# Optimization experiments

Measured on AMD Instinct MI355X. Metric: run time of the kernel, lower is better.

## Reference

```python
import jax, jax.numpy as jnp
import numpy as np

D_MODEL = 1024
H = 16
D_K = D_MODEL // H
D_FF = 4096
EPS = 1e-6
NEG = -1e9


def layer_norm(x, alpha, beta):
    # Custom LN: scalar alpha/beta, unbiased std, eps added to std (not var)
    mean = jnp.mean(x, axis=-1, keepdims=True)
    std = jnp.std(x, axis=-1, ddof=1, keepdims=True)
    return alpha * (x - mean) / (std + EPS) + beta


def setup_inputs() -> dict:
    key = jax.random.key(0)
    ks = jax.random.split(key, 16)
    B, S = 4, 2048
    s = 1.0 / np.sqrt(D_MODEL)
    inp = {
        "x": jax.random.normal(ks[0], (B, S, D_MODEL), dtype=jnp.float32),
        "src_mask": jax.random.randint(ks[1], (B, 1, 1, S), 0, 2, dtype=jnp.int32),
        "wq": jax.random.normal(ks[2], (D_MODEL, D_MODEL), jnp.float32) * s,
        "bq": jnp.zeros((D_MODEL,), jnp.float32),
        "wk": jax.random.normal(ks[3], (D_MODEL, D_MODEL), jnp.float32) * s,
        "bk": jnp.zeros((D_MODEL,), jnp.float32),
        "wv": jax.random.normal(ks[4], (D_MODEL, D_MODEL), jnp.float32) * s,
        "bv": jnp.zeros((D_MODEL,), jnp.float32),
        "wo": jax.random.normal(ks[5], (D_MODEL, D_MODEL), jnp.float32) * s,
        "bo": jnp.zeros((D_MODEL,), jnp.float32),
        "w1": jax.random.normal(ks[6], (D_MODEL, D_FF), jnp.float32) * s,
        "b1": jnp.zeros((D_FF,), jnp.float32),
        "w2": jax.random.normal(ks[7], (D_FF, D_MODEL), jnp.float32) * (1.0 / np.sqrt(D_FF)),
        "b2": jnp.zeros((D_MODEL,), jnp.float32),
        "a1": jnp.ones((1,), jnp.float32),
        "be1": jnp.zeros((1,), jnp.float32),
        "a2": jnp.ones((1,), jnp.float32),
        "be2": jnp.zeros((1,), jnp.float32),
    }
    return inp


def reference(x, src_mask, wq, bq, wk, bk, wv, bv, wo, bo, w1, b1, w2, b2, a1, be1, a2, be2):
    B, S, _ = x.shape

    # --- residual 1: self-attention on pre-LN input (dropout = identity, eval) ---
    xn = layer_norm(x, a1, be1)
    q = (xn @ wq + bq).reshape(B, S, H, D_K).transpose(0, 2, 1, 3)  # [B,H,S,Dk]
    k = (xn @ wk + bk).reshape(B, S, H, D_K).transpose(0, 2, 1, 3)
    v = (xn @ wv + bv).reshape(B, S, H, D_K).transpose(0, 2, 1, 3)

    scores = jnp.einsum("bhqd,bhkd->bhqk", q, k) / jnp.sqrt(jnp.float32(D_K))
    scores = jnp.where(src_mask == 0, jnp.float32(NEG), scores)
    attn = jax.nn.softmax(scores, axis=-1)
    ctx = jnp.einsum("bhqk,bhkd->bhqd", attn, v)  # [B,H,S,Dk]
    ctx = ctx.transpose(0, 2, 1, 3).reshape(B, S, D_MODEL)
    attn_out = ctx @ wo + bo
    x = x + attn_out

    # --- residual 2: feed-forward on pre-LN input ---
    xn2 = layer_norm(x, a2, be2)
    ff = jax.nn.relu(xn2 @ w1 + b1) @ w2 + b2
    return x + ff
```

## Files before the change

### kernel.cpp

```cpp
#include <hip/hip_runtime.h>
#include <stdint.h>

typedef unsigned short u16;
typedef __attribute__((ext_vector_type(8))) short short8;
typedef __attribute__((ext_vector_type(4))) float f32x4;
typedef __attribute__((ext_vector_type(4))) u16 u16x4;
typedef __attribute__((ext_vector_type(4))) uint32_t u32x4;

#define NB 4
#define SEQ 2048
#define DM 1024
#define NH 16
#define DKh 64
#define DFF 4096
#define LOG2E 1.44269504089f

__device__ __forceinline__ u16 f2bf(float f) {
  union { float f; uint32_t u; } v; v.f = f;
  uint32_t u = v.u;
  return (u16)((u + 0x7FFFu + ((u >> 16) & 1u)) >> 16);
}

__device__ __forceinline__ uint32_t cvtpk(float lo, float hi) {
  uint32_t r;
  asm("v_cvt_pk_bf16_f32 %0, %1, %2" : "=v"(r) : "v"(lo), "v"(hi));
  return r;
}

__device__ __forceinline__ float fexp2(float x) {
  float r;
  asm("v_exp_f32 %0, %1" : "=v"(r) : "v"(x));
  return r;
}

__device__ __forceinline__ void gl16(const u16* g, u16* l) {
  __builtin_amdgcn_global_load_lds((const __attribute__((address_space(1))) void*)g,
                                   (__attribute__((address_space(3))) void*)l, 16, 0, 0);
}

__global__ __launch_bounds__(256) void transpose4_bf16(const float* __restrict__ s0,
                                                       const float* __restrict__ s1,
                                                       const float* __restrict__ s2,
                                                       const float* __restrict__ s3,
                                                       u16* __restrict__ d0,
                                                       u16* __restrict__ d1,
                                                       u16* __restrict__ d2,
                                                       u16* __restrict__ d3) {
  __shared__ float tile[32][33];
  int z = blockIdx.z;
  const float* src = (z == 0) ? s0 : (z == 1) ? s1 : (z == 2) ? s2 : s3;
  u16* dst = (z == 0) ? d0 : (z == 1) ? d1 : (z == 2) ? d2 : d3;
  int tx = threadIdx.x, ty = threadIdx.y;
  int c0 = blockIdx.x * 32, r0 = blockIdx.y * 32;
#pragma unroll
  for (int i = 0; i < 32; i += 8)
    tile[ty + i][tx] = src[(size_t)(r0 + ty + i) * DM + c0 + tx];
  __syncthreads();
#pragma unroll
  for (int i = 0; i < 32; i += 8)
    dst[(size_t)(c0 + ty + i) * DM + r0 + tx] = f2bf(tile[tx][ty + i]);
}

__global__ __launch_bounds__(256) void transpose_bf16(const float* __restrict__ src,
                                                      u16* __restrict__ dst, int R, int C) {
  __shared__ float tile[32][33];
  int tx = threadIdx.x, ty = threadIdx.y;
  int c0 = blockIdx.x * 32, r0 = blockIdx.y * 32;
#pragma unroll
  for (int i = 0; i < 32; i += 8)
    tile[ty + i][tx] = src[(size_t)(r0 + ty + i) * C + c0 + tx];
  __syncthreads();
#pragma unroll
  for (int i = 0; i < 32; i += 8)
    dst[(size_t)(c0 + ty + i) * R + r0 + tx] = f2bf(tile[tx][ty + i]);
}

__global__ __launch_bounds__(256) void bias_cat(const float* __restrict__ bq,
                                                const float* __restrict__ bk,
                                                const float* __restrict__ bv,
                                                float* __restrict__ o) {
  int i = blockIdx.x * 256 + threadIdx.x;
  if (i < 3072) o[i] = (i < 1024) ? bq[i] : ((i < 2048) ? bk[i - 1024] : bv[i - 2048]);
}

__global__ __launch_bounds__(1024) void compact_idx(const int* __restrict__ msk,
                                                    int* __restrict__ pinv,
                                                    int* __restrict__ lArr,
                                                    int* __restrict__ lpArr,
                                                    float* __restrict__ fbbc) {
  int b = blockIdx.x;
  int t = threadIdx.x;
  int lane = t & 63, w = t >> 6;
  int i0 = t * 2, i1 = t * 2 + 1;
  int m0 = msk[b * SEQ + i0] ? 1 : 0;
  int m1 = msk[b * SEQ + i1] ? 1 : 0;
  int s = m0 + m1;
  int run = s;
#pragma unroll
  for (int d = 1; d < 64; d <<= 1) {
    int v = __shfl_up(run, d);
    if (lane >= d) run += v;
  }
  __shared__ int wtot[16];
  __shared__ int woff[17];
  if (lane == 63) wtot[w] = run;
  __syncthreads();
  if (t == 0) {
    int acc = 0;
#pragma unroll
    for (int i = 0; i < 16; ++i) { woff[i] = acc; acc += wtot[i]; }
    woff[16] = acc;
  }
  __syncthreads();
  int excl = run - s + woff[w];
  pinv[b * SEQ + i0] = m0 ? excl : -1;
  pinv[b * SEQ + i1] = m1 ? (excl + m0) : -1;
  int L = woff[16];
  if (t == 0) {
    lArr[b] = L;
    int LP = (L + 63) & ~63;
    if (LP == 0) LP = 64;
    lpArr[b] = LP;
  }
  for (int l = t; l < SEQ; l += 1024)
    fbbc[b * SEQ + l] = (l < L) ? 0.0f : -1e9f;
}

__global__ __launch_bounds__(256) void ln_bf16(const float* __restrict__ x,
                                               u16* __restrict__ out,
                                               const float* __restrict__ alpha,
                                               const float* __restrict__ beta) {
  int row = blockIdx.x;
  const float4* xr = (const float4*)(x + (size_t)row * DM);
  int t = threadIdx.x;
  float4 v = xr[t];
  float s = v.x + v.y + v.z + v.w;
  float s2 = v.x * v.x + v.y * v.y + v.z * v.z + v.w * v.w;
#pragma unroll
  for (int m = 1; m < 64; m <<= 1) { s += __shfl_xor(s, m); s2 += __shfl_xor(s2, m); }
  __shared__ float red[8];
  int wid = t >> 6, lane = t & 63;
  if (lane == 0) { red[wid] = s; red[wid + 4] = s2; }
  __syncthreads();
  float S = red[0] + red[1] + red[2] + red[3];
  float S2 = red[4] + red[5] + red[6] + red[7];
  float mean = S * (1.0f / DM);
  float var = fmaxf((S2 - S * mean) * (1.0f / (DM - 1)), 0.0f);
  float inv = alpha[0] / (sqrtf(var) + 1e-6f);
  float bet = beta[0];
  u16x4 o;
  o[0] = f2bf((v.x - mean) * inv + bet);
  o[1] = f2bf((v.y - mean) * inv + bet);
  o[2] = f2bf((v.z - mean) * inv + bet);
  o[3] = f2bf((v.w - mean) * inv + bet);
  *(u16x4*)(out + (size_t)row * DM + t * 4) = o;
}

template <int MODE>
__global__ __launch_bounds__(512, 4) void gemm_v2(const u16* __restrict__ A,
                                                  const u16* __restrict__ WT,
                                                  const float* __restrict__ bias,
                                                  const float* __restrict__ resid,
                                                  void* __restrict__ outp,
                                                  const int* __restrict__ pinv,
                                                  int M, int N, int K, float qscale) {
  extern __shared__ u16 lds[];
  int tid = threadIdx.x;
  int lane = tid & 63, wid = tid >> 6;
  int lr = lane & 15, lg = lane >> 4;
  int wr = wid >> 1, wc = wid & 1;
  int nbx = N >> 7;
  int nwg = (M >> 8) * nbx;
  int lid = blockIdx.x;
  int swz = (lid & 7) * (nwg >> 3) + (lid >> 3);
  int m0 = (swz / nbx) << 8, n0 = (swz % nbx) << 7;

  int sr = tid >> 2;
  int sch = tid & 3;
  int scs = sch ^ ((sr >> 1) & 3);
  size_t a_src = (size_t)(m0 + sr) * K + scs * 8;
  size_t b_src = (size_t)(n0 + sr) * K + scs * 8;
  u16* a_dst = lds + sr * 32 + sch * 8;
  u16* b_dst = lds + 8192 + sr * 32 + sch * 8;

#define STAGE(B_, T_) do { \
    gl16(A + a_src + (size_t)(T_) * 32, a_dst + (B_) * 12288); \
    gl16(A + a_src + (size_t)128 * K + (size_t)(T_) * 32, a_dst + (B_) * 12288 + 4096); \
    gl16(WT + b_src + (size_t)(T_) * 32, b_dst + (B_) * 12288); \
  } while (0)

  int rchunk = (lg ^ ((lr >> 1) & 3)) * 8;
  int offA[4], offB[4];
#pragma unroll
  for (int i = 0; i < 4; ++i) offA[i] = (wr * 64 + i * 16 + lr) * 32 + rchunk;
#pragma unroll
  for (int j = 0; j < 4; ++j) offB[j] = 8192 + (wc * 64 + j * 16 + lr) * 32 + rchunk;

  f32x4 acc[4][4] = {};

  int NT = K >> 5;
  STAGE(0, 0);
  STAGE(1, 1);
  asm volatile("s_waitcnt vmcnt(3)" ::: "memory");
  __builtin_amdgcn_s_barrier();

  int buf = 0;
  for (int t = 0; t < NT; ++t) {
    const u16* la = lds + buf * 12288;
    int b2 = buf - 1; if (b2 < 0) b2 += 3;
    short8 af[4], bfr[4];
#pragma unroll
    for (int i = 0; i < 4; ++i) af[i] = *(const short8*)&la[offA[i]];
#pragma unroll
    for (int j = 0; j < 4; ++j) bfr[j] = *(const short8*)&la[offB[j]];
    if (t + 2 < NT) STAGE(b2, t + 2);
    __builtin_amdgcn_s_setprio(1);
#pragma unroll
    for (int i = 0; i < 4; ++i)
#pragma unroll
      for (int j = 0; j < 4; ++j)
        acc[i][j] = __builtin_amdgcn_mfma_f32_16x16x32_bf16(af[i], bfr[j], acc[i][j], 0, 0, 0);
    __builtin_amdgcn_s_setprio(0);
    if (t < NT - 2) asm volatile("s_waitcnt vmcnt(3)" ::: "memory");
    else            asm volatile("s_waitcnt vmcnt(0)" ::: "memory");
    __builtin_amdgcn_s_barrier();
    __builtin_amdgcn_sched_barrier(0);
    buf = (buf == 2) ? 0 : buf + 1;
  }
#undef STAGE

#pragma unroll
  for (int i = 0; i < 4; ++i) {
#pragma unroll
    for (int j = 0; j < 4; ++j) {
      int col = n0 + wc * 64 + j * 16 + lr;
      float bi = bias[col];
      int rbase = m0 + wr * 64 + i * 16 + lg * 4;
      if (MODE == 2) {
        float* o = (float*)outp;
#pragma unroll
        for (int r = 0; r < 4; ++r) {
          size_t idx = (size_t)(rbase + r) * N + col;
          o[idx] = resid[idx] + acc[i][j][r] + bi;
        }
      } else if (MODE == 3) {
        u16* o = (u16*)outp;
#pragma unroll
        for (int r = 0; r < 4; ++r)
          o[(size_t)(rbase + r) * N + col] = f2bf(fmaxf(acc[i][j][r] + bi, 0.0f));
      } else {
        u16* qb = (u16*)outp;
        int which = col >> 10, nc = col & 1023;
        int hh = nc >> 6, dd = nc & 63;
        int bb = rbase >> 11, ss = rbase & 2047;
        if (which == 0) {
#pragma unroll
          for (int r = 0; r < 4; ++r)
            qb[((size_t)(bb * NH + hh) * SEQ + (ss + r)) * DKh + dd] = f2bf((acc[i][j][r] + bi) * qscale);
        } else {
          int4 p4 = *(const int4*)(pinv + bb * SEQ + ss);
          int pos[4] = {p4.x, p4.y, p4.z, p4.w};
          if (which == 1) {
            u16* kcb = qb + (size_t)(8u << 20);
#pragma unroll
            for (int r = 0; r < 4; ++r)
              if (pos[r] >= 0)
                kcb[((size_t)(bb * NH + hh) * SEQ + pos[r]) * DKh + dd] = f2bf(acc[i][j][r] + bi);
          } else {
            u16* vcb = qb + (size_t)2 * (8u << 20);
#pragma unroll
            for (int r = 0; r < 4; ++r)
              if (pos[r] >= 0) {
                int l = pos[r];
                int lo = l & 63;
                int pi = ((lo >> 4) & 1) * 32 + ((lo >> 2) & 3) * 8 + (lo >> 5) * 4 + (lo & 3);
                vcb[((size_t)(bb * NH + hh) * DKh + dd) * SEQ + (l & ~63) + pi] = f2bf(acc[i][j][r] + bi);
              }
          }
        }
      }
    }
  }
}

__global__ __launch_bounds__(256) void attn_fwd(const u16* __restrict__ q,
                                                const u16* __restrict__ kc,
                                                const u16* __restrict__ vc,
                                                const int* __restrict__ lArr,
                                                const int* __restrict__ lpArr,
                                                const float* __restrict__ fbbc,
                                                u16* __restrict__ ctx) {
  __shared__ u16 lds[2][8192];
  int tid = threadIdx.x;
  int wid = tid >> 6, lane = tid & 63;
  int lr = lane & 15, lg = lane >> 4;
  int bh = blockIdx.x;
  int b = bh >> 4, hh = bh & 15;
  int q0 = blockIdx.y * 128;
  const u16* qbase = q + (size_t)bh * SEQ * DKh;
  const u16* kcb = kc + (size_t)bh * SEQ * DKh;
  const u16* vcb = vc + (size_t)bh * DKh * SEQ;
  const float* fbbase = fbbc + b * SEQ;
  int Lb = lArr[b];
  int LP = lpArr[b];

  short8 qf[2][2];
#pragma unroll
  for (int i = 0; i < 2; ++i)
#pragma unroll
    for (int kk = 0; kk < 2; ++kk)
      qf[i][kk] = *(const short8*)(qbase + (size_t)(q0 + wid * 32 + i * 16 + lr) * DKh + kk * 32 + lg * 8);

  int srow = tid >> 3;
  int schk = tid & 7;
  int ks0 = srow * 64 + ((schk ^ (srow & 7)) * 8);
  int vs0 = srow * SEQ + ((schk ^ (srow & 7)) * 8);
  int dst0 = tid * 8;

#define STAGE(B_, KV0) do { \
    gl16(kcb + (size_t)(KV0) * 64 + ks0, &lds[B_][dst0]); \
    gl16(kcb + (size_t)(KV0) * 64 + ks0 + 2048, &lds[B_][dst0 + 2048]); \
    gl16(vcb + (size_t)(KV0) + vs0, &lds[B_][dst0 + 4096]); \
    gl16(vcb + (size_t)(KV0) + vs0 + 32 * SEQ, &lds[B_][dst0 + 6144]); \
  } while (0)

  int swzc = (lr & 7) << 3;

  f32x4 ot[2][4] = {};
  float mrow[2] = {-3e38f, -3e38f};
  float lsum[2] = {0.0f, 0.0f};

  STAGE(0, 0);
  __syncthreads();

  int buf = 0;
  for (int kv0 = 0; kv0 < LP; kv0 += 64) {
    if (kv0 + 64 < LP) STAGE(buf ^ 1, kv0 + 64);
    const u16* Ks = lds[buf];
    const u16* Vs = lds[buf] + 4096;

    f32x4 st[2][4] = {};
    __builtin_amdgcn_s_setprio(1);
#pragma unroll
    for (int kk = 0; kk < 2; ++kk) {
      short8 kf[4];
#pragma unroll
      for (int j = 0; j < 4; ++j)
        kf[j] = *(const short8*)&Ks[(j * 16 + lr) * 64 + ((kk * 32 + lg * 8) ^ swzc)];
#pragma unroll
      for (int i = 0; i < 2; ++i)
#pragma unroll
        for (int j = 0; j < 4; ++j)
          st[i][j] = __builtin_amdgcn_mfma_f32_16x16x32_bf16(kf[j], qf[i][kk], st[i][j], 0, 0, 0);
    }
    __builtin_amdgcn_s_setprio(0);

    bool tail = (kv0 + 64 > Lb);

    u32x4 pa[2][2];
#pragma unroll
    for (int i = 0; i < 2; ++i) {
      float p[4][4];
      if (tail) {
#pragma unroll
        for (int j = 0; j < 4; ++j) {
          float4 f4 = *(const float4*)(fbbase + kv0 + j * 16 + lg * 4);
          p[j][0] = st[i][j][0] + f4.x;
          p[j][1] = st[i][j][1] + f4.y;
          p[j][2] = st[i][j][2] + f4.z;
          p[j][3] = st[i][j][3] + f4.w;
        }
      } else {
#pragma unroll
        for (int j = 0; j < 4; ++j)
#pragma unroll
          for (int r = 0; r < 4; ++r) p[j][r] = st[i][j][r];
      }
      float mx = -3e38f;
#pragma unroll
      for (int j = 0; j < 4; ++j)
#pragma unroll
        for (int r = 0; r < 4; ++r) mx = fmaxf(mx, p[j][r]);
      mx = fmaxf(mx, __shfl_xor(mx, 16));
      mx = fmaxf(mx, __shfl_xor(mx, 32));
      float mnew = fmaxf(mrow[i], mx);
      if (!__all(mnew - mrow[i] <= 8.0f)) {
        float corr = fexp2(mrow[i] - mnew);
        lsum[i] *= corr;
#pragma unroll
        for (int jd = 0; jd < 4; ++jd)
#pragma unroll
          for (int r = 0; r < 4; ++r) ot[i][jd][r] *= corr;
        mrow[i] = mnew;
      }
      float ps = 0.0f;
#pragma unroll
      for (int j = 0; j < 4; ++j)
#pragma unroll
        for (int r = 0; r < 4; ++r) {
          float pv = fexp2(p[j][r] - mrow[i]);
          p[j][r] = pv;
          ps += pv;
        }
      ps += __shfl_xor(ps, 16);
      ps += __shfl_xor(ps, 32);
      lsum[i] += ps;
#pragma unroll
      for (int ks = 0; ks < 2; ++ks) {
        pa[i][ks][0] = cvtpk(p[ks][0], p[ks][1]);
        pa[i][ks][1] = cvtpk(p[ks][2], p[ks][3]);
        pa[i][ks][2] = cvtpk(p[ks + 2][0], p[ks + 2][1]);
        pa[i][ks][3] = cvtpk(p[ks + 2][2], p[ks + 2][3]);
      }
    }

    __builtin_amdgcn_s_setprio(1);
#pragma unroll
    for (int ks = 0; ks < 2; ++ks) {
      short8 vf[4];
#pragma unroll
      for (int jd = 0; jd < 4; ++jd)
        vf[jd] = *(const short8*)&Vs[(jd * 16 + lr) * 64 + ((ks * 32 + lg * 8) ^ swzc)];
#pragma unroll
      for (int i = 0; i < 2; ++i)
#pragma unroll
        for (int jd = 0; jd < 4; ++jd)
          ot[i][jd] = __builtin_amdgcn_mfma_f32_16x16x32_bf16(vf[jd], *(short8*)&pa[i][ks], ot[i][jd], 0, 0, 0);
    }
    __builtin_amdgcn_s_setprio(0);
    __syncthreads();
    buf ^= 1;
  }
#undef STAGE

  float inv0 = 1.0f / lsum[0], inv1 = 1.0f / lsum[1];
  u16* ep = &lds[0][wid * 2048];
#pragma unroll
  for (int i = 0; i < 2; ++i) {
    float inv = i ? inv1 : inv0;
#pragma unroll
    for (int jd = 0; jd < 4; ++jd) {
      uint32_t w0 = cvtpk(ot[i][jd][0] * inv, ot[i][jd][1] * inv);
      uint32_t w1 = cvtpk(ot[i][jd][2] * inv, ot[i][jd][3] * inv);
      uint32_t pk2[2] = {w0, w1};
      *(u16x4*)&ep[(i * 16 + lr) * 64 + ((jd * 16 + lg * 4) ^ swzc)] = *(u16x4*)pk2;
    }
  }
  __syncthreads();
  int q_ = lane >> 1;
  size_t orow = ((size_t)b * SEQ + q0 + wid * 32 + q_) * DM + hh * DKh;
#pragma unroll
  for (int it = 0; it < 4; ++it) {
    int dc = (lane & 1) * 32 + it * 8;
    short8 vv = *(const short8*)&ep[q_ * 64 + (dc ^ ((q_ & 7) << 3))];
    *(short8*)(ctx + orow + dc) = vv;
  }
}

extern "C" void kernel_launch(void* const* d_in, const int* in_sizes, int n_in,
                              void* d_out, int out_size, void* d_ws, size_t ws_size,
                              hipStream_t stream) {
  const float* x   = (const float*)d_in[0];
  const int*   msk = (const int*)d_in[1];
  const float* wq  = (const float*)d_in[2];
  const float* bq  = (const float*)d_in[3];
  const float* wk  = (const float*)d_in[4];
  const float* bk  = (const float*)d_in[5];
  const float* wv  = (const float*)d_in[6];
  const float* bv  = (const float*)d_in[7];
  const float* wo  = (const float*)d_in[8];
  const float* bo  = (const float*)d_in[9];
  const float* w1  = (const float*)d_in[10];
  const float* b1  = (const float*)d_in[11];
  const float* w2  = (const float*)d_in[12];
  const float* b2  = (const float*)d_in[13];
  const float* a1  = (const float*)d_in[14];
  const float* be1 = (const float*)d_in[15];
  const float* a2  = (const float*)d_in[16];
  const float* be2 = (const float*)d_in[17];
  float* out = (float*)d_out;

  u16* wqT = (u16*)d_ws;
  u16* wkT = wqT + (1u << 20);
  u16* wvT = wkT + (1u << 20);
  u16* woT = wvT + (1u << 20);
  u16* w1T = woT + (1u << 20);
  u16* w2T = w1T + (4u << 20);
  u16* xn  = w2T + (4u << 20);
  u16* qb  = xn  + (8u << 20);
  u16* kb  = qb  + (8u << 20);
  u16* vtb = kb  + (8u << 20);
  u16* ctx = vtb + (8u << 20);
  u16* hb  = qb;
  float* bcat = (float*)ctx;
  int*   pinv = (int*)(ctx + (8u << 20));
  int*   lArr = pinv + NB * SEQ;
  int*   lpArr = lArr + 16;
  float* fbbc = (float*)(lpArr + 16);

  (void)hipFuncSetAttribute((const void*)gemm_v2<0>, hipFuncAttributeMaxDynamicSharedMemorySize, 72 * 1024);
  (void)hipFuncSetAttribute((const void*)gemm_v2<2>, hipFuncAttributeMaxDynamicSharedMemorySize, 72 * 1024);
  (void)hipFuncSetAttribute((const void*)gemm_v2<3>, hipFuncAttributeMaxDynamicSharedMemorySize, 72 * 1024);

  dim3 tb(32, 8);
  transpose4_bf16<<<dim3(32, 32, 4), tb, 0, stream>>>(wq, wk, wv, wo, wqT, wkT, wvT, woT);
  transpose_bf16<<<dim3(128, 32), tb, 0, stream>>>(w1, w1T, DM, DFF);
  transpose_bf16<<<dim3(32, 128), tb, 0, stream>>>(w2, w2T, DFF, DM);
  bias_cat<<<12, 256, 0, stream>>>(bq, bk, bv, bcat);
  compact_idx<<<NB, 1024, 0, stream>>>(msk, pinv, lArr, lpArr, fbbc);

  ln_bf16<<<NB * SEQ, 256, 0, stream>>>(x, xn, a1, be1);

  gemm_v2<0><<<768, 512, 72 * 1024, stream>>>(xn, wqT, bcat, nullptr, qb, pinv, NB * SEQ, 3 * DM, DM, 0.125f * LOG2E);

  attn_fwd<<<dim3(NB * NH, SEQ / 128), 256, 0, stream>>>(qb, kb, vtb, lArr, lpArr, fbbc, ctx);

  gemm_v2<2><<<256, 512, 72 * 1024, stream>>>(ctx, woT, bo, x, out, nullptr, NB * SEQ, DM, DM, 1.0f);

  ln_bf16<<<NB * SEQ, 256, 0, stream>>>(out, xn, a2, be2);

  gemm_v2<3><<<1024, 512, 72 * 1024, stream>>>(xn, w1T, b1, nullptr, hb, nullptr, NB * SEQ, DFF, DM, 1.0f);

  gemm_v2<2><<<256, 512, 72 * 1024, stream>>>(hb, w2T, b2, out, out, nullptr, NB * SEQ, DM, DFF, 1.0f);
}
```

Baseline: 353.9 us.

## Enlarge attention blocks to 256 queries with 128-key stages and explicit waitcnt

The attention kernel now runs 8 waves per block covering 256 query rows, and stages 128 keys/values per double-buffered LDS step instead of 64. Each K/V tile loaded from global memory is therefore shared by twice as many query rows. The __syncthreads calls are replaced by explicit vmcnt waits plus barriers, so the prefetch of the next stage stays in flight during compute. In exchange the block uses 64KB of LDS, which lowers occupancy, and there are half as many blocks. The loop advances by 128 keys, so it relies on LP being a multiple of 128 or on masked padding being valid for the tail sub-block.

Result: no change. 349.3 us (median of 2 runs) (-1.3%).

```diff
diff --git a/kernel.cpp b/kernel.cpp
--- a/kernel.cpp
+++ b/kernel.cpp
@@ -283,20 +283,20 @@
   }
 }
 
-__global__ __launch_bounds__(256) void attn_fwd(const u16* __restrict__ q,
+__global__ __launch_bounds__(512) void attn_fwd(const u16* __restrict__ q,
                                                 const u16* __restrict__ kc,
                                                 const u16* __restrict__ vc,
                                                 const int* __restrict__ lArr,
                                                 const int* __restrict__ lpArr,
                                                 const float* __restrict__ fbbc,
                                                 u16* __restrict__ ctx) {
-  __shared__ u16 lds[2][8192];
+  __shared__ u16 lds[2][16384];
   int tid = threadIdx.x;
   int wid = tid >> 6, lane = tid & 63;
   int lr = lane & 15, lg = lane >> 4;
   int bh = blockIdx.x;
   int b = bh >> 4, hh = bh & 15;
-  int q0 = blockIdx.y * 128;
+  int q0 = blockIdx.y * 256 + wid * 32;
   const u16* qbase = q + (size_t)bh * SEQ * DKh;
   const u16* kcb = kc + (size_t)bh * SEQ * DKh;
   const u16* vcb = vc + (size_t)bh * DKh * SEQ;
@@ -309,7 +309,7 @@
   for (int i = 0; i < 2; ++i)
 #pragma unroll
     for (int kk = 0; kk < 2; ++kk)
-      qf[i][kk] = *(const short8*)(qbase + (size_t)(q0 + wid * 32 + i * 16 + lr) * DKh + kk * 32 + lg * 8);
+      qf[i][kk] = *(const short8*)(qbase + (size_t)(q0 + i * 16 + lr) * DKh + kk * 32 + lg * 8);
 
   int srow = tid >> 3;
   int schk = tid & 7;
@@ -319,9 +319,9 @@
 
 #define STAGE(B_, KV0) do { \
     gl16(kcb + (size_t)(KV0) * 64 + ks0, &lds[B_][dst0]); \
-    gl16(kcb + (size_t)(KV0) * 64 + ks0 + 2048, &lds[B_][dst0 + 2048]); \
-    gl16(vcb + (size_t)(KV0) + vs0, &lds[B_][dst0 + 4096]); \
-    gl16(vcb + (size_t)(KV0) + vs0 + 32 * SEQ, &lds[B_][dst0 + 6144]); \
+    gl16(kcb + (size_t)((KV0) + 64) * 64 + ks0, &lds[B_][dst0 + 4096]); \
+    gl16(vcb + (size_t)(KV0) + vs0, &lds[B_][dst0 + 8192]); \
+    gl16(vcb + (size_t)(KV0) + 64 + vs0, &lds[B_][dst0 + 12288]); \
   } while (0)
 
   int swzc = (lr & 7) << 3;
@@ -331,107 +331,120 @@
   float lsum[2] = {0.0f, 0.0f};
 
   STAGE(0, 0);
-  __syncthreads();
+  asm volatile("s_waitcnt vmcnt(0)" ::: "memory");
+  __builtin_amdgcn_s_barrier();
 
   int buf = 0;
-  for (int kv0 = 0; kv0 < LP; kv0 += 64) {
-    if (kv0 + 64 < LP) STAGE(buf ^ 1, kv0 + 64);
-    const u16* Ks = lds[buf];
-    const u16* Vs = lds[buf] + 4096;
-
-    f32x4 st[2][4] = {};
-    __builtin_amdgcn_s_setprio(1);
-#pragma unroll
-    for (int kk = 0; kk < 2; ++kk) {
-      short8 kf[4];
-#pragma unroll
-      for (int j = 0; j < 4; ++j)
-        kf[j] = *(const short8*)&Ks[(j * 16 + lr) * 64 + ((kk * 32 + lg * 8) ^ swzc)];
-#pragma unroll
-      for (int i = 0; i < 2; ++i)
+  for (int kv0 = 0; kv0 < LP; kv0 += 128) {
+    bool more = (kv0 + 128 < LP);
+    if (more) STAGE(buf ^ 1, kv0 + 128);
+    if (more) asm volatile("s_waitcnt vmcnt(4)" ::: "memory");
+    else      asm volatile("s_waitcnt vmcnt(0)" ::: "memory");
+    __builtin_amdgcn_s_barrier();
+
+#pragma unroll
+    for (int sB = 0; sB < 2; ++sB) {
+      const u16* Ks = &lds[buf][sB * 4096];
+      const u16* Vs = &lds[buf][8192 + sB * 4096];
+      int kvs = kv0 + sB * 64;
+
+      f32x4 st[2][4] = {};
+      __builtin_amdgcn_s_setprio(1);
+#pragma unroll
+      for (int kk = 0; kk < 2; ++kk) {
+        short8 kf[4];
 #pragma unroll
         for (int j = 0; j < 4; ++j)
-          st[i][j] = __builtin_amdgcn_mfma_f32_16x16x32_bf16(kf[j], qf[i][kk], st[i][j], 0, 0, 0);
+          kf[j] = *(const short8*)&Ks[(j * 16 + lr) * 64 + ((kk * 32 + lg * 8) ^ swzc)];
+#pragma unroll
+        for (int i = 0; i < 2; ++i)
+#pragma unroll
+          for (int j = 0; j < 4; ++j)
+            st[i][j] = __builtin_amdgcn_mfma_f32_16x16x32_bf16(kf[j], qf[i][kk], st[i][j], 0, 0, 0);
+      }
+      __builtin_amdgcn_s_setprio(0);
+
+      bool tail = (kvs + 64 > Lb);
+
+      u32x4 pa[2][2];
+#pragma unroll
+      for (int i = 0; i < 2; ++i) {
+        float p[4][4];
+        if (tail) {
+#pragma unroll
+          for (int j = 0; j < 4; ++j) {
+            float4 f4 = *(const float4*)(fbbase + kvs + j * 16 + lg * 4);
+            p[j][0] = st[i][j][0] + f4.x;
+            p[j][1] = st[i][j][1] + f4.y;
+            p[j][2] = st[i][j][2] + f4.z;
+            p[j][3] = st[i][j][3] + f4.w;
+          }
+        } else {
+#pragma unroll
+          for (int j = 0; j < 4; ++j)
+#pragma unroll
+            for (int r = 0; r < 4; ++r) p[j][r] = st[i][j][r];
+        }
+        float mx = -3e38f;
+#pragma unroll
+        for (int j = 0; j < 4; ++j)
+#pragma unroll
+          for (int r = 0; r < 4; ++r) mx = fmaxf(mx, p[j][r]);
+        mx = fmaxf(mx, __shfl_xor(mx, 16));
+        mx = fmaxf(mx, __shfl_xor(mx, 32));
+        float mnew = fmaxf(mrow[i], mx);
+        if (!__all(mnew - mrow[i] <= 8.0f)) {
+          float corr = fexp2(mrow[i] - mnew);
+          lsum[i] *= corr;
+#pragma unroll
+          for (int jd = 0; jd < 4; ++jd)
+#pragma unroll
+            for (int r = 0; r < 4; ++r) ot[i][jd][r] *= corr;
+          mrow[i] = mnew;
+        }
+        float ps = 0.0f;
+#pragma unroll
+        for (int j = 0; j < 4; ++j)
+#pragma unroll
+          for (int r = 0; r < 4; ++r) {
+            float pv = fexp2(p[j][r] - mrow[i]);
+            p[j][r] = pv;
+            ps += pv;
+          }
+        ps += __shfl_xor(ps, 16);
+        ps += __shfl_xor(ps, 32);
+        lsum[i] += ps;
+#pragma unroll
+        for (int ks = 0; ks < 2; ++ks) {
+          pa[i][ks][0] = cvtpk(p[ks][0], p[ks][1]);
+          pa[i][ks][1] = cvtpk(p[ks][2], p[ks][3]);
+          pa[i][ks][2] = cvtpk(p[ks + 2][0], p[ks + 2][1]);
+          pa[i][ks][3] = cvtpk(p[ks + 2][2], p[ks + 2][3]);
+        }
+      }
+
+      __builtin_amdgcn_s_setprio(1);
+#pragma unroll
+      for (int ks = 0; ks < 2; ++ks) {
+        short8 vf[4];
+#pragma unroll
+        for (int jd = 0; jd < 4; ++jd)
+          vf[jd] = *(const short8*)&Vs[(jd * 16 + lr) * 64 + ((ks * 32 + lg * 8) ^ swzc)];
+#pragma unroll
+        for (int i = 0; i < 2; ++i)
+#pragma unroll
+          for (int jd = 0; jd < 4; ++jd)
+            ot[i][jd] = __builtin_amdgcn_mfma_f32_16x16x32_bf16(vf[jd], *(short8*)&pa[i][ks], ot[i][jd], 0, 0, 0);
+      }
+      __builtin_amdgcn_s_setprio(0);
     }
-    __builtin_amdgcn_s_setprio(0);
-
-    bool tail = (kv0 + 64 > Lb);
-
-    u32x4 pa[2][2];
-#pragma unroll
-    for (int i = 0; i < 2; ++i) {
-      float p[4][4];
-      if (tail) {
-#pragma unroll
-        for (int j = 0; j < 4; ++j) {
-          float4 f4 = *(const float4*)(fbbase + kv0 + j * 16 + lg * 4);
-          p[j][0] = st[i][j][0] + f4.x;
-          p[j][1] = st[i][j][1] + f4.y;
-          p[j][2] = st[i][j][2] + f4.z;
-          p[j][3] = st[i][j][3] + f4.w;
-        }
-      } else {
-#pragma unroll
-        for (int j = 0; j < 4; ++j)
-#pragma unroll
-          for (int r = 0; r < 4; ++r) p[j][r] = st[i][j][r];
-      }
-      float mx = -3e38f;
-#pragma unroll
-      for (int j = 0; j < 4; ++j)
-#pragma unroll
-        for (int r = 0; r < 4; ++r) mx = fmaxf(mx, p[j][r]);
-      mx = fmaxf(mx, __shfl_xor(mx, 16));
-      mx = fmaxf(mx, __shfl_xor(mx, 32));
-      float mnew = fmaxf(mrow[i], mx);
-      if (!__all(mnew - mrow[i] <= 8.0f)) {
-        float corr = fexp2(mrow[i] - mnew);
-        lsum[i] *= corr;
-#pragma unroll
-        for (int jd = 0; jd < 4; ++jd)
-#pragma unroll
-          for (int r = 0; r < 4; ++r) ot[i][jd][r] *= corr;
-        mrow[i] = mnew;
-      }
-      float ps = 0.0f;
-#pragma unroll
-      for (int j = 0; j < 4; ++j)
-#pragma unroll
-        for (int r = 0; r < 4; ++r) {
-          float pv = fexp2(p[j][r] - mrow[i]);
-          p[j][r] = pv;
-          ps += pv;
-        }
-      ps += __shfl_xor(ps, 16);
-      ps += __shfl_xor(ps, 32);
-      lsum[i] += ps;
-#pragma unroll
-      for (int ks = 0; ks < 2; ++ks) {
-        pa[i][ks][0] = cvtpk(p[ks][0], p[ks][1]);
-        pa[i][ks][1] = cvtpk(p[ks][2], p[ks][3]);
-        pa[i][ks][2] = cvtpk(p[ks + 2][0], p[ks + 2][1]);
-        pa[i][ks][3] = cvtpk(p[ks + 2][2], p[ks + 2][3]);
-      }
-    }
-
-    __builtin_amdgcn_s_setprio(1);
-#pragma unroll
-    for (int ks = 0; ks < 2; ++ks) {
-      short8 vf[4];
-#pragma unroll
-      for (int jd = 0; jd < 4; ++jd)
-        vf[jd] = *(const short8*)&Vs[(jd * 16 + lr) * 64 + ((ks * 32 + lg * 8) ^ swzc)];
-#pragma unroll
-      for (int i = 0; i < 2; ++i)
-#pragma unroll
-        for (int jd = 0; jd < 4; ++jd)
-          ot[i][jd] = __builtin_amdgcn_mfma_f32_16x16x32_bf16(vf[jd], *(short8*)&pa[i][ks], ot[i][jd], 0, 0, 0);
-    }
-    __builtin_amdgcn_s_setprio(0);
-    __syncthreads();
+    __builtin_amdgcn_s_barrier();
     buf ^= 1;
   }
 #undef STAGE
+
+  asm volatile("s_waitcnt vmcnt(0)" ::: "memory");
+  __builtin_amdgcn_s_barrier();
 
   float inv0 = 1.0f / lsum[0], inv1 = 1.0f / lsum[1];
   u16* ep = &lds[0][wid * 2048];
@@ -448,7 +461,7 @@
   }
   __syncthreads();
   int q_ = lane >> 1;
-  size_t orow = ((size_t)b * SEQ + q0 + wid * 32 + q_) * DM + hh * DKh;
+  size_t orow = ((size_t)b * SEQ + q0 + q_) * DM + hh * DKh;
 #pragma unroll
   for (int it = 0; it < 4; ++it) {
     int dc = (lane & 1) * 32 + it * 8;
@@ -513,7 +526,7 @@
 
   gemm_v2<0><<<768, 512, 72 * 1024, stream>>>(xn, wqT, bcat, nullptr, qb, pinv, NB * SEQ, 3 * DM, DM, 0.125f * LOG2E);
 
-  attn_fwd<<<dim3(NB * NH, SEQ / 128), 256, 0, stream>>>(qb, kb, vtb, lArr, lpArr, fbbc, ctx);
+  attn_fwd<<<dim3(NB * NH, SEQ / 256), 512, 0, stream>>>(qb, kb, vtb, lArr, lpArr, fbbc, ctx);
 
   gemm_v2<2><<<256, 512, 72 * 1024, stream>>>(ctx, woT, bo, x, out, nullptr, NB * SEQ, DM, DM, 1.0f);
 
```
